# Optimization experiments

Hardware: AMD Instinct MI355X
Metric: run time of the kernel (lower is better)

## Reference

```python
import jax, jax.numpy as jnp
import numpy as np

D_MODEL = 1024
N_HEADS = 16
D_HEAD = D_MODEL // N_HEADS
ROPE_BASE = 10000.0


def _rotate_half(x):
    half = x.shape[-1] // 2
    x1, x2 = x[..., :half], x[..., half:]
    return jnp.concatenate([-x2, x1], axis=-1)


def _rope_cos_sin(seq_len, d_head, dtype):
    inv_freq = 1.0 / (ROPE_BASE ** (jnp.arange(0, d_head, 2, dtype=jnp.float32) / d_head))
    t = jnp.arange(seq_len, dtype=jnp.float32)
    freqs = jnp.outer(t, inv_freq)                       # [S, d_head/2]
    emb = jnp.concatenate([freqs, freqs], axis=-1)       # [S, d_head]
    return jnp.cos(emb).astype(dtype), jnp.sin(emb).astype(dtype)


def setup_inputs() -> dict:
    key = jax.random.key(0)
    k1, k2, k3 = jax.random.split(key, 3)
    B, S = 2, 2048
    x = jax.random.normal(k1, (B, S, D_MODEL), dtype=jnp.float32)
    # torch nn.Linear weight layout: [out_features, in_features], y = x @ W.T
    w_qkv = jax.random.normal(k2, (3 * D_MODEL, D_MODEL), dtype=jnp.float32) * (D_MODEL ** -0.5)
    w_out = jax.random.normal(k3, (D_MODEL, D_MODEL), dtype=jnp.float32) * (D_MODEL ** -0.5)
    return {"x": x, "w_qkv": w_qkv, "w_out": w_out}


def reference(x, w_qkv, w_out):
    B, S, _ = x.shape
    qkv = jnp.einsum('bsd,ed->bse', x, w_qkv)            # [B, S, 3*D]
    qkv = qkv.reshape(B, S, 3, N_HEADS, D_HEAD)
    qkv = jnp.transpose(qkv, (2, 0, 3, 1, 4))            # [3, B, H, S, Dh]
    q, k, v = qkv[0], qkv[1], qkv[2]

    cos, sin = _rope_cos_sin(S, D_HEAD, x.dtype)         # [S, Dh] each
    cos = cos[None, None]                                # [1, 1, S, Dh]
    sin = sin[None, None]
    q = q * cos + _rotate_half(q) * sin
    k = k * cos + _rotate_half(k) * sin

    scale = 1.0 / jnp.sqrt(jnp.array(D_HEAD, dtype=x.dtype))
    attn = jnp.einsum('bhqd,bhkd->bhqk', q, k) * scale   # [B, H, S, S]
    causal = jnp.tril(jnp.ones((S, S), dtype=bool))      # triu(diag=1) masked -> keep lower tri
    attn = jnp.where(causal[None, None], attn, jnp.finfo(x.dtype).min)
    attn = jax.nn.softmax(attn, axis=-1)

    out = jnp.einsum('bhqk,bhkd->bhqd', attn, v)         # [B, H, S, Dh]
    out = jnp.transpose(out, (0, 2, 1, 3)).reshape(B, S, D_MODEL)
    return jnp.einsum('bsd,ed->bse', out, w_out)         # out_proj
```

## Files before the change

### kernel.cpp

```cpp
#include <hip/hip_runtime.h>
#include <hip/hip_bf16.h>
#include <cmath>

#define DMODEL 1024
#define NH 16
#define DH 64
#define SEQ 2048
#define BATCH 2

typedef __attribute__((ext_vector_type(8))) short bf16x8;
typedef __attribute__((ext_vector_type(4))) float f32x4;
typedef __attribute__((ext_vector_type(4))) unsigned int u32x4;
typedef __attribute__((ext_vector_type(8))) unsigned short u16x8;

typedef __attribute__((address_space(3))) unsigned int lds_u32;
typedef const __attribute__((address_space(1))) unsigned int g_u32;

__device__ __forceinline__ unsigned short f2bf(float f) {
    unsigned int u = __builtin_bit_cast(unsigned int, f);
    u += 0x7fffu + ((u >> 16) & 1u);
    return (unsigned short)(u >> 16);
}
__device__ __forceinline__ float exp2_fast(float x) {
    float r;
    asm("v_exp_f32 %0, %1" : "=v"(r) : "v"(x));
    return r;
}

__global__ __launch_bounds__(256)
void cast_all(const float* __restrict__ x, const float* __restrict__ wq,
              const float* __restrict__ wo, unsigned short* __restrict__ xb,
              unsigned short* __restrict__ wqb, unsigned short* __restrict__ wob)
{
    const int i = blockIdx.x * 256 + threadIdx.x;
    const float* src; unsigned short* dst; int off;
    if (i < 524288)      { src = x;  dst = xb;  off = i; }
    else if (i < 917504) { src = wq; dst = wqb; off = i - 524288; }
    else                 { src = wo; dst = wob; off = i - 917504; }
    const float4 a = *(const float4*)(src + (size_t)off * 8);
    const float4 b = *(const float4*)(src + (size_t)off * 8 + 4);
    u16x8 o;
    o[0] = f2bf(a.x); o[1] = f2bf(a.y); o[2] = f2bf(a.z); o[3] = f2bf(a.w);
    o[4] = f2bf(b.x); o[5] = f2bf(b.y); o[6] = f2bf(b.z); o[7] = f2bf(b.w);
    *(u16x8*)(dst + (size_t)off * 8) = o;
}

__global__ __launch_bounds__(512, 4)
void gemm_qkv(const unsigned short* __restrict__ A,
              const unsigned short* __restrict__ B,
              unsigned short* __restrict__ oq, unsigned short* __restrict__ ok,
              unsigned short* __restrict__ ovt)
{
    constexpr int K = 1024;
    constexpr int BK = 32;
    constexpr int NT = K / BK;
    __shared__ unsigned short As[2][128 * BK];
    __shared__ unsigned short Bs[2][256 * BK];

    const int t  = threadIdx.x;
    const int l  = t & 63;
    const int w  = t >> 6;
    const int g  = l >> 4;
    const int ln = l & 15;
    const int wr = w >> 2;
    const int wc = w & 3;
    const int m0 = blockIdx.y * 128;
    const int n0 = blockIdx.x * 256;

    auto stage = [&](int kt, int bufi) {
        {
            const int r = t >> 2, slot = t & 3;
            const int kk = kt * BK + ((slot ^ ((r >> 1) & 3)) * 8);
            const unsigned short* ga = A + (size_t)(m0 + r) * K + kk;
            __builtin_amdgcn_global_load_lds((g_u32*)ga,
                (lds_u32*)&As[bufi][t * 8], 16, 0, 0);
        }
        #pragma unroll
        for (int i = 0; i < 2; ++i) {
            const int n = i * 512 + t;
            const int r = n >> 2, slot = n & 3;
            const int kk = kt * BK + ((slot ^ ((r >> 1) & 3)) * 8);
            const unsigned short* gb = B + (size_t)(n0 + r) * K + kk;
            __builtin_amdgcn_global_load_lds((g_u32*)gb,
                (lds_u32*)&Bs[bufi][n * 8], 16, 0, 0);
        }
    };

    f32x4 acc[4][4];
    #pragma unroll
    for (int i = 0; i < 4; ++i)
        #pragma unroll
        for (int j = 0; j < 4; ++j) acc[i][j] = (f32x4){0.f, 0.f, 0.f, 0.f};

    const int swz = (g ^ ((ln >> 1) & 3)) << 4;

    stage(0, 0);
    for (int kt = 0; kt < NT; ++kt) {
        __syncthreads();
        if (kt + 1 < NT) stage(kt + 1, (kt + 1) & 1);
        const char* as = (const char*)As[kt & 1];
        const char* bs = (const char*)Bs[kt & 1];
        bf16x8 af[4], bfr[4];
        #pragma unroll
        for (int fm = 0; fm < 4; ++fm)
            af[fm] = *(const bf16x8*)(as + (wr * 64 + fm * 16 + ln) * 64 + swz);
        #pragma unroll
        for (int fn = 0; fn < 4; ++fn)
            bfr[fn] = *(const bf16x8*)(bs + (wc * 64 + fn * 16 + ln) * 64 + swz);
        #pragma unroll
        for (int fm = 0; fm < 4; ++fm)
            #pragma unroll
            for (int fn = 0; fn < 4; ++fn)
                acc[fm][fn] = __builtin_amdgcn_mfma_f32_16x16x32_bf16(
                    af[fm], bfr[fn], acc[fm][fn], 0, 0, 0);
    }

    const int rowbase = m0 + wr * 64;
    const int chead = n0 + wc * 64;
    const int which = chead >> 10;
    const int h = (chead >> 6) & (NH - 1);
    if (which < 2) {
        unsigned short* dst = which == 0 ? oq : ok;
        const float scale = which == 0 ? 0.18033688011112042f : 1.f;
        const float cexp = -13.287712379549449f / 32.f;
        const float if0 = exp2f((float)ln * cexp);
        const float if1 = exp2f((float)(16 + ln) * cexp);
        #pragma unroll
        for (int fm = 0; fm < 4; ++fm)
            #pragma unroll
            for (int rr = 0; rr < 4; ++rr) {
                const int row = rowbase + fm * 16 + g * 4 + rr;
                const int b = row >> 11, s = row & (SEQ - 1);
                float s0, c0, s1, c1;
                __sincosf((float)s * if0, &s0, &c0);
                __sincosf((float)s * if1, &s1, &c1);
                const float x0 = acc[fm][0][rr], x1 = acc[fm][1][rr];
                const float x2 = acc[fm][2][rr], x3 = acc[fm][3][rr];
                const size_t base = (((size_t)b * NH + h) * SEQ + s) * DH;
                dst[base + ln]      = f2bf((x0 * c0 - x2 * s0) * scale);
                dst[base + 16 + ln] = f2bf((x1 * c1 - x3 * s1) * scale);
                dst[base + 32 + ln] = f2bf((x2 * c0 + x0 * s0) * scale);
                dst[base + 48 + ln] = f2bf((x3 * c1 + x1 * s1) * scale);
            }
    } else {
        #pragma unroll
        for (int fm = 0; fm < 4; ++fm)
            #pragma unroll
            for (int fn = 0; fn < 4; ++fn) {
                const int row = rowbase + fm * 16 + g * 4;
                const int b = row >> 11, s = row & (SEQ - 1);
                const int d = fn * 16 + ln;
                ushort4 pk;
                pk.x = f2bf(acc[fm][fn][0]); pk.y = f2bf(acc[fm][fn][1]);
                pk.z = f2bf(acc[fm][fn][2]); pk.w = f2bf(acc[fm][fn][3]);
                *(ushort4*)&ovt[(((size_t)b * NH + h) * DH + d) * SEQ + s] = pk;
            }
    }
}

__global__ __launch_bounds__(256)
void gemm_out(const unsigned short* __restrict__ A,
              const unsigned short* __restrict__ B,
              float* __restrict__ oc, int M, int N)
{
    constexpr int K = 1024;
    constexpr int BK = 32;
    constexpr int NT = K / BK;
    constexpr int BM = 64;
    constexpr int FM = 2;
    __shared__ unsigned short As[2][BM * BK];
    __shared__ unsigned short Bs[2][128 * BK];

    const int t  = threadIdx.x;
    const int l  = t & 63;
    const int w  = t >> 6;
    const int g  = l >> 4;
    const int ln = l & 15;
    const int wr = w >> 1, wc = w & 1;
    const int m0 = blockIdx.y * BM;
    const int n0 = blockIdx.x * 128;

    auto stage = [&](int kt, int bufi) {
        {
            const int r = t >> 2, slot = t & 3;
            const int kk = kt * BK + ((slot ^ ((r >> 1) & 3)) * 8);
            const unsigned short* ga = A + (size_t)(m0 + r) * K + kk;
            __builtin_amdgcn_global_load_lds((g_u32*)ga,
                (lds_u32*)&As[bufi][t * 8], 16, 0, 0);
        }
        #pragma unroll
        for (int i = 0; i < 2; ++i) {
            const int n = i * 256 + t;
            const int r = n >> 2, slot = n & 3;
            const int kk = kt * BK + ((slot ^ ((r >> 1) & 3)) * 8);
            const unsigned short* gb = B + (size_t)(n0 + r) * K + kk;
            __builtin_amdgcn_global_load_lds((g_u32*)gb,
                (lds_u32*)&Bs[bufi][n * 8], 16, 0, 0);
        }
    };

    f32x4 acc[FM][4];
    #pragma unroll
    for (int i = 0; i < FM; ++i)
        #pragma unroll
        for (int j = 0; j < 4; ++j) acc[i][j] = (f32x4){0.f, 0.f, 0.f, 0.f};

    const int swz = (g ^ ((ln >> 1) & 3)) << 4;

    stage(0, 0);
    for (int kt = 0; kt < NT; ++kt) {
        __syncthreads();
        if (kt + 1 < NT) stage(kt + 1, (kt + 1) & 1);
        const char* as = (const char*)As[kt & 1];
        const char* bs = (const char*)Bs[kt & 1];
        bf16x8 af[FM], bfr[4];
        #pragma unroll
        for (int fm = 0; fm < FM; ++fm)
            af[fm] = *(const bf16x8*)(as + (wr * (BM / 2) + fm * 16 + ln) * 64 + swz);
        #pragma unroll
        for (int fn = 0; fn < 4; ++fn)
            bfr[fn] = *(const bf16x8*)(bs + (wc * 64 + fn * 16 + ln) * 64 + swz);
        #pragma unroll
        for (int fm = 0; fm < FM; ++fm)
            #pragma unroll
            for (int fn = 0; fn < 4; ++fn)
                acc[fm][fn] = __builtin_amdgcn_mfma_f32_16x16x32_bf16(
                    af[fm], bfr[fn], acc[fm][fn], 0, 0, 0);
    }

    const int rowbase = m0 + wr * (BM / 2);
    const int colbase = n0 + wc * 64;
    #pragma unroll
    for (int fm = 0; fm < FM; ++fm)
        #pragma unroll
        for (int fn = 0; fn < 4; ++fn)
            #pragma unroll
            for (int rr = 0; rr < 4; ++rr) {
                const int row = rowbase + fm * 16 + g * 4 + rr;
                oc[(size_t)row * N + colbase + fn * 16 + ln] = acc[fm][fn][rr];
            }
}

__global__ __launch_bounds__(512, 4)
void attn_mfma(const unsigned short* __restrict__ q,
               const unsigned short* __restrict__ k,
               const unsigned short* __restrict__ vt,
               unsigned short* __restrict__ ob)
{
    __shared__ unsigned short Ks[2][64 * 64];
    __shared__ unsigned short Vs[2][64 * 64];

    const int t  = threadIdx.x;
    const int l  = t & 63;
    const int w  = t >> 6;
    const int wq = w & 3;
    const int g  = l >> 4;
    const int ln = l & 15;
    const int bid = blockIdx.x;
    const int xcd = bid & 7, jj = bid >> 3;
    const int bh = xcd * 4 + (jj >> 4);
    const int pi = jj & 15;
    const int qtA = pi, qtB = 31 - pi;
    const int myqt = (w < 4) ? qtA : qtB;
    const size_t bqk = (size_t)bh * SEQ * DH;
    const size_t bv  = (size_t)bh * DH * SEQ;

    bf16x8 qf0, qf1;
    {
        const unsigned short* qp = q + bqk + (size_t)(myqt * 64 + wq * 16 + ln) * DH + g * 8;
        qf0 = *(const bf16x8*)qp;
        qf1 = *(const bf16x8*)(qp + 32);
    }

    f32x4 ao[4];
    #pragma unroll
    for (int i = 0; i < 4; ++i) ao[i] = (f32x4){0.f, 0.f, 0.f, 0.f};
    float l_ = 0.f;

    auto stage = [&](int kt, int bufi) {
        const int row = t >> 3, sl = t & 7;
        const int sg  = (row & 3) | (((row >> 3) & 1) << 2);
        const int slg = (sl ^ sg) * 8;
        const unsigned short* gk = k  + bqk + (size_t)(kt * 64 + row) * DH + slg;
        const unsigned short* gv = vt + bv  + (size_t)row * SEQ + kt * 64 + slg;
        __builtin_amdgcn_global_load_lds((g_u32*)gk,
            (lds_u32*)&Ks[bufi][t * 8], 16, 0, 0);
        __builtin_amdgcn_global_load_lds((g_u32*)gv,
            (lds_u32*)&Vs[bufi][t * 8], 16, 0, 0);
    };

    const int rowoffK = ((ln >> 2) * 8 + (ln & 3)) * 128;
    const int sK = (ln & 3) | (((ln >> 2) & 1) << 2);
    const int slotK0 = ((g ^ sK) << 4);
    const int slotK1 = (((g + 4) ^ sK) << 4);
    const int sV = (ln & 3) | (((ln >> 3) & 1) << 2);

    stage(0, 0);
    for (int kt = 0; kt <= qtB; ++kt) {
        __syncthreads();
        if (kt < qtB) stage(kt + 1, (kt + 1) & 1);
        const bool act = (kt <= myqt);
        const char* kb = (const char*)Ks[kt & 1];
        const char* vb = (const char*)Vs[kt & 1];

        if (act) {
            f32x4 s[4];
            #pragma unroll
            for (int nb = 0; nb < 4; ++nb) s[nb] = (f32x4){0.f, 0.f, 0.f, 0.f};

            __builtin_amdgcn_s_setprio(1);
            #pragma unroll
            for (int nb = 0; nb < 4; ++nb) {
                const char* kr = kb + ((nb >> 1) * 32 + (nb & 1) * 4) * 128 + rowoffK;
                bf16x8 kf0 = *(const bf16x8*)(kr + slotK0);
                bf16x8 kf1 = *(const bf16x8*)(kr + slotK1);
                s[nb] = __builtin_amdgcn_mfma_f32_16x16x32_bf16(kf0, qf0, s[nb], 0, 0, 0);
                s[nb] = __builtin_amdgcn_mfma_f32_16x16x32_bf16(kf1, qf1, s[nb], 0, 0, 0);
            }
            __builtin_amdgcn_s_setprio(0);

            bf16x8 vf[8];
            #pragma unroll
            for (int ks = 0; ks < 2; ++ks)
                #pragma unroll
                for (int db = 0; db < 4; ++db) {
                    const int d = db * 16 + ln;
                    vf[ks * 4 + db] = *(const bf16x8*)(vb + d * 128 + (((ks * 4 + g) ^ sV) << 4));
                }

            if (kt == myqt) {
                #pragma unroll
                for (int nb = 0; nb < 4; ++nb)
                    #pragma unroll
                    for (int r = 0; r < 4; ++r)
                        if ((nb >> 1) * 32 + g * 8 + (nb & 1) * 4 + r > wq * 16 + ln)
                            s[nb][r] = -INFINITY;
            }

            const float M2 = 28.853900817779268f;
            bf16x8 pf[2];
            {
                float rs = 0.f;
                unsigned int dw[8];
                #pragma unroll
                for (int nb = 0; nb < 4; ++nb) {
                    float e[4];
                    #pragma unroll
                    for (int r = 0; r < 4; ++r)
                        e[r] = exp2_fast(s[nb][r] - M2);
                    rs += (e[0] + e[1]) + (e[2] + e[3]);
                    dw[nb * 2] = __builtin_amdgcn_perm(
                        __builtin_bit_cast(unsigned int, e[1]),
                        __builtin_bit_cast(unsigned int, e[0]), 0x07060302u);
                    dw[nb * 2 + 1] = __builtin_amdgcn_perm(
                        __builtin_bit_cast(unsigned int, e[3]),
                        __builtin_bit_cast(unsigned int, e[2]), 0x07060302u);
                }
                l_ += rs;
                pf[0] = __builtin_bit_cast(bf16x8, (u32x4){dw[0], dw[1], dw[2], dw[3]});
                pf[1] = __builtin_bit_cast(bf16x8, (u32x4){dw[4], dw[5], dw[6], dw[7]});
            }

            __builtin_amdgcn_s_setprio(1);
            #pragma unroll
            for (int ks = 0; ks < 2; ++ks)
                #pragma unroll
                for (int db = 0; db < 4; ++db)
                    ao[db] = __builtin_amdgcn_mfma_f32_16x16x32_bf16(
                        pf[ks], vf[ks * 4 + db], ao[db], 0, 0, 0);
            __builtin_amdgcn_s_setprio(0);
        }
    }

    l_ += __shfl_xor(l_, 16); l_ += __shfl_xor(l_, 32);
    const int b = bh >> 4, h = bh & (NH - 1);
    const float inv = 1.f / l_;
    #pragma unroll
    for (int r = 0; r < 4; ++r) {
        const float iv = __shfl(inv, g * 4 + r);
        const size_t row = (size_t)(b * SEQ + myqt * 64 + wq * 16 + g * 4 + r) * DMODEL + h * DH;
        #pragma unroll
        for (int db = 0; db < 4; ++db)
            ob[row + db * 16 + ln] = f2bf(ao[db][r] * iv);
    }
}

extern "C" void kernel_launch(void* const* d_in, const int* in_sizes, int n_in,
                              void* d_out, int out_size, void* d_ws, size_t ws_size,
                              hipStream_t stream)
{
    const float* x  = (const float*)d_in[0];
    const float* wq = (const float*)d_in[1];
    const float* wo = (const float*)d_in[2];
    float* out = (float*)d_out;

    const size_t NQ = (size_t)BATCH * NH * SEQ * DH;
    unsigned short* qb  = (unsigned short*)d_ws;
    unsigned short* kb  = qb + NQ;
    unsigned short* vtb = kb + NQ;
    unsigned short* ob  = vtb + NQ;
    unsigned short* xb  = ob + NQ;
    unsigned short* wqb = xb + NQ;
    unsigned short* wob = wqb + 3 * DMODEL * DMODEL;

    cast_all<<<4096, 256, 0, stream>>>(x, wq, wo, xb, wqb, wob);

    dim3 g1(3072 / 256, 4096 / 128);
    gemm_qkv<<<g1, 512, 0, stream>>>(xb, wqb, qb, kb, vtb);

    attn_mfma<<<512, 512, 0, stream>>>(qb, kb, vtb, ob);

    dim3 g3(1024 / 128, 4096 / 64);
    gemm_out<<<g3, 256, 0, stream>>>(ob, wob, out, 4096, 1024);
}
```

Baseline: 102.7 us.

## Enlarge QKV GEMM tile to 256x256 with BK=64 and phased async staging

Rewrites the QKV projection GEMM main loop to use a 256x256 output tile per block and a K step of 64 instead of 128x256 with a K step of 32. Global-to-LDS loads are split into four phases that are interleaved with the MFMA sub-steps, using explicit vmcnt waits, raw barriers and s_setprio around the MFMA bursts. The aim is more operand reuse per LDS load, fewer barriers per K, and better overlap of loads with math. In exchange it doubles LDS and register use (launch bounds lowered to 2 blocks per CU) and halves the grid to 192 blocks, which is fewer than the number of CUs.

Result: no change. 103.2 us (+0.6%).

```diff
diff --git a/kernel.cpp b/kernel.cpp
--- a/kernel.cpp
+++ b/kernel.cpp
@@ -45,17 +45,15 @@
     *(u16x8*)(dst + (size_t)off * 8) = o;
 }
 
-__global__ __launch_bounds__(512, 4)
+__global__ __launch_bounds__(512, 2)
 void gemm_qkv(const unsigned short* __restrict__ A,
               const unsigned short* __restrict__ B,
               unsigned short* __restrict__ oq, unsigned short* __restrict__ ok,
               unsigned short* __restrict__ ovt)
 {
     constexpr int K = 1024;
-    constexpr int BK = 32;
-    constexpr int NT = K / BK;
-    __shared__ unsigned short As[2][128 * BK];
-    __shared__ unsigned short Bs[2][256 * BK];
+    __shared__ unsigned short As[2][256 * 64];
+    __shared__ unsigned short Bs[2][256 * 64];
 
     const int t  = threadIdx.x;
     const int l  = t & 63;
@@ -64,58 +62,95 @@
     const int ln = l & 15;
     const int wr = w >> 2;
     const int wc = w & 3;
-    const int m0 = blockIdx.y * 128;
+    const int m0 = blockIdx.y * 256;
     const int n0 = blockIdx.x * 256;
 
-    auto stage = [&](int kt, int bufi) {
-        {
-            const int r = t >> 2, slot = t & 3;
-            const int kk = kt * BK + ((slot ^ ((r >> 1) & 3)) * 8);
-            const unsigned short* ga = A + (size_t)(m0 + r) * K + kk;
-            __builtin_amdgcn_global_load_lds((g_u32*)ga,
-                (lds_u32*)&As[bufi][t * 8], 16, 0, 0);
+    const int r0 = t >> 3;
+    const int r1 = 64 + r0;
+    const int sl = t & 7;
+    const int sg0 = (sl ^ (r0 & 7)) * 8;
+    const int sg1 = (sl ^ (r1 & 7)) * 8;
+
+    auto stage = [&](int tn, int ph) {
+        const int mat = ph >> 1, half = ph & 1;
+        const int buf = tn & 1;
+        const unsigned short* gsrc = (mat == 0) ? A : B;
+        unsigned short* lb = (mat == 0) ? &As[buf][0] : &Bs[buf][0];
+        const int base = ((mat == 0) ? m0 : n0) + half * 128;
+        const int kk = tn * 64;
+        const unsigned short* g0 = gsrc + (size_t)(base + r0) * K + kk + sg0;
+        const unsigned short* g1 = gsrc + (size_t)(base + r1) * K + kk + sg1;
+        __builtin_amdgcn_global_load_lds((g_u32*)g0,
+            (lds_u32*)(lb + half * 8192 + t * 8), 16, 0, 0);
+        __builtin_amdgcn_global_load_lds((g_u32*)g1,
+            (lds_u32*)(lb + half * 8192 + (512 + t) * 8), 16, 0, 0);
+    };
+
+    f32x4 acc[8][4];
+    #pragma unroll
+    for (int i = 0; i < 8; ++i)
+        #pragma unroll
+        for (int j = 0; j < 4; ++j) acc[i][j] = (f32x4){0.f, 0.f, 0.f, 0.f};
+
+    stage(0, 0); stage(0, 1); stage(0, 2); stage(0, 3);
+
+    for (int i = 0; i < 8; ++i) {
+        bf16x8 aq[4][2];
+        #pragma unroll
+        for (int p = 0; p < 8; ++p) {
+            const int mh = (p >> 1) & 1;
+            const int nh = p & 1;
+            const int cbuf = (p < 4) ? 0 : 1;
+            const int tn = (p < 4) ? (2 * i + 1)
+                                   : ((2 * i + 2 > 15) ? 14 : (2 * i + 2));
+            if (p == 0 || p == 4) {
+                __builtin_amdgcn_s_barrier();
+                asm volatile("" ::: "memory");
+                stage(tn, p & 3);
+                asm volatile("s_waitcnt vmcnt(2)" ::: "memory");
+                __builtin_amdgcn_s_barrier();
+                asm volatile("" ::: "memory");
+            } else {
+                stage(tn, p & 3);
+            }
+
+            const char* as = (const char*)As[cbuf];
+            const char* bs = (const char*)Bs[cbuf];
+            if (nh == 0) {
+                #pragma unroll
+                for (int fm = 0; fm < 4; ++fm) {
+                    const int row = wr * 128 + mh * 64 + fm * 16 + ln;
+                    #pragma unroll
+                    for (int ks = 0; ks < 2; ++ks)
+                        aq[fm][ks] = *(const bf16x8*)(as + row * 128 +
+                            (((g + ks * 4) ^ (row & 7)) << 4));
+                }
+            }
+            bf16x8 bq[2][2];
+            #pragma unroll
+            for (int fn = 0; fn < 2; ++fn) {
+                const int row = wc * 64 + nh * 32 + fn * 16 + ln;
+                #pragma unroll
+                for (int ks = 0; ks < 2; ++ks)
+                    bq[fn][ks] = *(const bf16x8*)(bs + row * 128 +
+                        (((g + ks * 4) ^ (row & 7)) << 4));
+            }
+            __builtin_amdgcn_s_setprio(1);
+            #pragma unroll
+            for (int fm = 0; fm < 4; ++fm)
+                #pragma unroll
+                for (int fn = 0; fn < 2; ++fn)
+                    #pragma unroll
+                    for (int ks = 0; ks < 2; ++ks)
+                        acc[mh * 4 + fm][nh * 2 + fn] =
+                            __builtin_amdgcn_mfma_f32_16x16x32_bf16(
+                                aq[fm][ks], bq[fn][ks],
+                                acc[mh * 4 + fm][nh * 2 + fn], 0, 0, 0);
+            __builtin_amdgcn_s_setprio(0);
         }
-        #pragma unroll
-        for (int i = 0; i < 2; ++i) {
-            const int n = i * 512 + t;
-            const int r = n >> 2, slot = n & 3;
-            const int kk = kt * BK + ((slot ^ ((r >> 1) & 3)) * 8);
-            const unsigned short* gb = B + (size_t)(n0 + r) * K + kk;
-            __builtin_amdgcn_global_load_lds((g_u32*)gb,
-                (lds_u32*)&Bs[bufi][n * 8], 16, 0, 0);
-        }
-    };
-
-    f32x4 acc[4][4];
-    #pragma unroll
-    for (int i = 0; i < 4; ++i)
-        #pragma unroll
-        for (int j = 0; j < 4; ++j) acc[i][j] = (f32x4){0.f, 0.f, 0.f, 0.f};
-
-    const int swz = (g ^ ((ln >> 1) & 3)) << 4;
-
-    stage(0, 0);
-    for (int kt = 0; kt < NT; ++kt) {
-        __syncthreads();
-        if (kt + 1 < NT) stage(kt + 1, (kt + 1) & 1);
-        const char* as = (const char*)As[kt & 1];
-        const char* bs = (const char*)Bs[kt & 1];
-        bf16x8 af[4], bfr[4];
-        #pragma unroll
-        for (int fm = 0; fm < 4; ++fm)
-            af[fm] = *(const bf16x8*)(as + (wr * 64 + fm * 16 + ln) * 64 + swz);
-        #pragma unroll
-        for (int fn = 0; fn < 4; ++fn)
-            bfr[fn] = *(const bf16x8*)(bs + (wc * 64 + fn * 16 + ln) * 64 + swz);
-        #pragma unroll
-        for (int fm = 0; fm < 4; ++fm)
-            #pragma unroll
-            for (int fn = 0; fn < 4; ++fn)
-                acc[fm][fn] = __builtin_amdgcn_mfma_f32_16x16x32_bf16(
-                    af[fm], bfr[fn], acc[fm][fn], 0, 0, 0);
-    }
-
-    const int rowbase = m0 + wr * 64;
+    }
+
+    const int rowbase = m0 + wr * 128;
     const int chead = n0 + wc * 64;
     const int which = chead >> 10;
     const int h = (chead >> 6) & (NH - 1);
@@ -126,7 +161,7 @@
         const float if0 = exp2f((float)ln * cexp);
         const float if1 = exp2f((float)(16 + ln) * cexp);
         #pragma unroll
-        for (int fm = 0; fm < 4; ++fm)
+        for (int fm = 0; fm < 8; ++fm)
             #pragma unroll
             for (int rr = 0; rr < 4; ++rr) {
                 const int row = rowbase + fm * 16 + g * 4 + rr;
@@ -144,7 +179,7 @@
             }
     } else {
         #pragma unroll
-        for (int fm = 0; fm < 4; ++fm)
+        for (int fm = 0; fm < 8; ++fm)
             #pragma unroll
             for (int fn = 0; fn < 4; ++fn) {
                 const int row = rowbase + fm * 16 + g * 4;
@@ -405,7 +440,7 @@
 
     cast_all<<<4096, 256, 0, stream>>>(x, wq, wo, xb, wqb, wob);
 
-    dim3 g1(3072 / 256, 4096 / 128);
+    dim3 g1(3072 / 256, 4096 / 256);
     gemm_qkv<<<g1, 512, 0, stream>>>(xb, wqb, qb, kb, vtb);
 
     attn_mfma<<<512, 512, 0, stream>>>(qb, kb, vtb, ob);
```
